# Optimization experiments

Measured on AMD Instinct MI355X. Metric: run time of the kernel, lower is better.

Reference implementation:

```python
import jax, jax.numpy as jnp
import numpy as np

THRESHOLD = 6.2
N_SECTIONS = 9      # n_conv_sections
SEC_LEN = 4         # n_section_length
SEC_H = 9           # n_input_sections + n_section_length - 1
BATCH = 16384


def setup_inputs() -> dict:
    key = jax.random.key(0)
    k1, k2 = jax.random.split(key)
    # input spike-wave tensor [T, C=1, H=41, W=40]
    x = jax.random.uniform(k1, (BATCH, 1, 41, 40), dtype=jnp.float32)
    # per-section conv weights, N(0.8, 0.05) as in snn.Convolution init
    W = 0.8 + 0.05 * jax.random.normal(k2, (N_SECTIONS, 50, 1, 6, 40), dtype=jnp.float32)
    return {"x": x, "W": W}


def _conv(sec, w):
    # sec: [B,1,9,40], w: [50,1,6,40] -> [B,50,4,1]
    return jax.lax.conv_general_dilated(
        sec, w, window_strides=(1, 1), padding='VALID',
        dimension_numbers=('NCHW', 'OIHW', 'NCHW'))


def reference(x, W):
    # slice the 9 overlapping input sections -> [9, B, 1, 9, 40]
    sec = jnp.stack([x[:, :, i * SEC_LEN:i * SEC_LEN + SEC_H, :]
                     for i in range(N_SECTIONS)])
    pots = jax.vmap(_conv)(sec, W)                      # [9, B, 50, 4, 1]
    pots = jnp.max(pots, axis=3, keepdims=True)         # Pooling((4,1)) -> [9, B, 50, 1, 1]
    spks = jnp.where(pots > THRESHOLD, 1.0, 0.0).astype(pots.dtype)
    # concat sections along height (dim=2 of [B,C,H,W])
    pots_cat = jnp.moveaxis(pots[:, :, :, 0, :], 0, 2)  # [B, 50, 9, 1]
    spks_cat = jnp.moveaxis(spks[:, :, :, 0, :], 0, 2)  # [B, 50, 9, 1]
    return pots_cat, spks_cat
```

## Files before the change

kernel.cpp:

```cpp
#include <hip/hip_runtime.h>
#include <cstdint>
#include <cstddef>

#define NBATCH   16384
#define NSEC     9
#define NOC      50
#define NOCP     64
#define KPAD     256
#define KREAL    240
#define XROW     1640
#define XSF      1664
#define TB       16
#define OUTHALF  7372800
#define THRESH   6.2f

typedef _Float16 half8  __attribute__((ext_vector_type(8)));
typedef float    f32x4  __attribute__((ext_vector_type(4)));

__device__ inline half8 cvt8(float4 a, float4 b) {
    half8 h;
    h[0] = (_Float16)a.x; h[1] = (_Float16)a.y;
    h[2] = (_Float16)a.z; h[3] = (_Float16)a.w;
    h[4] = (_Float16)b.x; h[5] = (_Float16)b.y;
    h[6] = (_Float16)b.z; h[7] = (_Float16)b.w;
    return h;
}

__device__ inline void stg_load(const float* __restrict__ xrow, int u,
                                float4& a, float4& b) {
    if (u < 205) {
        a = *(const float4*)(xrow + u * 8);
        b = *(const float4*)(xrow + u * 8 + 4);
    } else {
        a = float4{0, 0, 0, 0};
        b = float4{0, 0, 0, 0};
    }
}

__device__ inline void stg_write(_Float16* lrow, int u, int ssw,
                                 float4 a, float4 b) {
    *(half8*)(lrow + ((u ^ ssw) << 3)) = cvt8(a, b);
}

__global__ __launch_bounds__(256)
void wconv_kernel(const float* __restrict__ W, _Float16* __restrict__ wks) {
    int idx = blockIdx.x * 256 + threadIdx.x;
    int k   = idx & 255;
    int ocp = (idx >> 8) & 63;
    int sec = idx >> 14;
    float v = 0.0f;
    if (ocp < NOC && k < KREAL)
        v = W[(size_t)(sec * NOC + ocp) * KREAL + k];
    wks[idx] = (_Float16)v;
}

__global__ __launch_bounds__(256, 2)
void fused_kernel(const float* __restrict__ x,
                  const _Float16* __restrict__ wks,
                  float* __restrict__ out) {
    __shared__ __align__(16) _Float16 xs[TB * XSF];

    const int tid = threadIdx.x;
    const size_t b0 = (size_t)blockIdx.x * TB;

    const int bb  = tid >> 4;
    const int u16 = tid & 15;
    const int ssw = bb & 7;
    const float* xrow = x + (b0 + bb) * XROW;
    _Float16* lrow = xs + bb * XSF;

    const int lane  = tid & 63;
    const int w     = tid >> 6;
    const int l15   = lane & 15;
    const int quad  = lane >> 4;
    const int mbase = 8 * (w >> 1);
    const int nbase = 32 * (w & 1);

    const int row0 = mbase + (l15 >> 2);
    const int row1 = row0 + 4;
    const _Float16* arow0 = xs + row0 * XSF;
    const _Float16* arow1 = xs + row1 * XSF;
    const int sw0 = row0 & 7;
    const int sw1 = row1 & 7;
    const int ubase = (l15 & 3) * 5 + quad;

    const _Float16* wb = wks + (size_t)(nbase + l15) * KPAD + quad * 8;

    half8 bv0[2][4], bv1[2][4];
    f32x4 acc00, acc01, acc10, acc11;
    float res[NSEC][2][2];

#define BPREF(ss, hh, B) { \
    const _Float16* wsec_ = wb + (size_t)((ss) * NOCP) * KPAD + (hh) * 128; \
    B[0][0] = *(const half8*)(wsec_);                \
    B[0][1] = *(const half8*)(wsec_ + 32);           \
    B[0][2] = *(const half8*)(wsec_ + 64);           \
    B[0][3] = *(const half8*)(wsec_ + 96);           \
    B[1][0] = *(const half8*)(wsec_ + 16 * KPAD);        \
    B[1][1] = *(const half8*)(wsec_ + 16 * KPAD + 32);   \
    B[1][2] = *(const half8*)(wsec_ + 16 * KPAD + 64);   \
    B[1][3] = *(const half8*)(wsec_ + 16 * KPAD + 96);   \
}

#define CHALF(ss, hh, B) { \
    _Pragma("unroll") \
    for (int kk = 0; kk < 4; ++kk) { \
        const int unit_ = (ss) * 20 + ((hh) * 4 + kk) * 4 + ubase; \
        half8 av0_ = *(const half8*)(arow0 + ((unit_ ^ sw0) << 3)); \
        half8 av1_ = *(const half8*)(arow1 + ((unit_ ^ sw1) << 3)); \
        acc00 = __builtin_amdgcn_mfma_f32_16x16x32_f16(av0_, B[0][kk], acc00, 0, 0, 0); \
        acc01 = __builtin_amdgcn_mfma_f32_16x16x32_f16(av0_, B[1][kk], acc01, 0, 0, 0); \
        acc10 = __builtin_amdgcn_mfma_f32_16x16x32_f16(av1_, B[0][kk], acc10, 0, 0, 0); \
        acc11 = __builtin_amdgcn_mfma_f32_16x16x32_f16(av1_, B[1][kk], acc11, 0, 0, 0); \
    } \
}

#define SECTION(ss) { \
    BPREF(ss, 1, bv1); \
    acc00 = f32x4{}; acc01 = f32x4{}; acc10 = f32x4{}; acc11 = f32x4{}; \
    CHALF(ss, 0, bv0); \
    if ((ss) < 8) BPREF((ss) + 1, 0, bv0); \
    CHALF(ss, 1, bv1); \
    res[ss][0][0] = fmaxf(fmaxf(acc00[0], acc00[1]), fmaxf(acc00[2], acc00[3])); \
    res[ss][0][1] = fmaxf(fmaxf(acc01[0], acc01[1]), fmaxf(acc01[2], acc01[3])); \
    res[ss][1][0] = fmaxf(fmaxf(acc10[0], acc10[1]), fmaxf(acc10[2], acc10[3])); \
    res[ss][1][1] = fmaxf(fmaxf(acc11[0], acc11[1]), fmaxf(acc11[2], acc11[3])); \
}

    {
        #pragma unroll
        for (int c = 0; c < 2; ++c) {
            const int jn = c ? 6 : 7;
            float4 va[7], vb[7];
            #pragma unroll
            for (int jj = 0; jj < 7; ++jj)
                if (jj < jn)
                    stg_load(xrow, u16 + 16 * (c * 7 + jj), va[jj], vb[jj]);
            if (c == 0) BPREF(0, 0, bv0);
            #pragma unroll
            for (int jj = 0; jj < 7; ++jj)
                if (jj < jn)
                    stg_write(lrow, u16 + 16 * (c * 7 + jj), ssw, va[jj], vb[jj]);
        }
    }
    __syncthreads();

    SECTION(0);
    SECTION(1);
    SECTION(2);
    SECTION(3);
    SECTION(4);
    SECTION(5);
    SECTION(6);
    SECTION(7);
    SECTION(8);

    __syncthreads();
    float* tb = (float*)xs;
    #pragma unroll
    for (int mt = 0; mt < 2; ++mt) {
        const int bl = mbase + 4 * mt + quad;
        #pragma unroll
        for (int nt = 0; nt < 2; ++nt) {
            const int oc = nbase + nt * 16 + l15;
            if (oc < NOC) {
                #pragma unroll
                for (int s = 0; s < NSEC; ++s)
                    tb[bl * 450 + oc * 9 + s] = res[s][mt][nt];
            }
        }
    }
    __syncthreads();

    const size_t ob = b0 * 450;
    const float4* t4 = (const float4*)tb;
    float4* o4  = (float4*)(out + ob);
    float4* o4s = (float4*)(out + OUTHALF + ob);
    for (int i = tid; i < TB * 450 / 4; i += 256) {
        float4 v = t4[i];
        o4[i] = v;
        float4 sp;
        sp.x = (v.x > THRESH) ? 1.0f : 0.0f;
        sp.y = (v.y > THRESH) ? 1.0f : 0.0f;
        sp.z = (v.z > THRESH) ? 1.0f : 0.0f;
        sp.w = (v.w > THRESH) ? 1.0f : 0.0f;
        o4s[i] = sp;
    }
}

__global__ __launch_bounds__(256)
void naive_kernel(const float* __restrict__ x, const float* __restrict__ W,
                  float* __restrict__ out) {
    size_t idx = (size_t)blockIdx.x * 256 + threadIdx.x;
    if (idx >= OUTHALF) return;
    int s  = (int)(idx % NSEC);
    int oc = (int)((idx / NSEC) % NOC);
    int b  = (int)(idx / (NSEC * NOC));
    const float* xb = x + (size_t)b * XROW + s * 160;
    const float* wv = W + (size_t)(s * NOC + oc) * KREAL;
    float best = -1e30f;
    for (int h0 = 0; h0 < 4; ++h0) {
        float acc = 0.0f;
        for (int k = 0; k < KREAL; ++k)
            acc += xb[h0 * 40 + k] * wv[k];
        best = fmaxf(best, acc);
    }
    out[idx] = best;
    out[OUTHALF + idx] = (best > THRESH) ? 1.0f : 0.0f;
}

extern "C" void kernel_launch(void* const* d_in, const int* in_sizes, int n_in,
                              void* d_out, int out_size, void* d_ws, size_t ws_size,
                              hipStream_t stream) {
    const float* x = (const float*)d_in[0];
    const float* W = (const float*)d_in[1];
    float* out = (float*)d_out;

    const size_t w_bytes = (size_t)NSEC * NOCP * KPAD * sizeof(_Float16);

    if (ws_size < w_bytes) {
        naive_kernel<<<(OUTHALF + 255) / 256, 256, 0, stream>>>(x, W, out);
        return;
    }

    _Float16* wks = (_Float16*)d_ws;

    wconv_kernel<<<(NSEC * NOCP * KPAD) / 256, 256, 0, stream>>>(W, wks);
    fused_kernel<<<NBATCH / TB, 256, 0, stream>>>(x, wks, out);
}
```

Measured before the change: 229.8 us.

## Halve batch tile to 8 and split waves by output-channel block

Reduces the per-block batch tile from 16 to 8 samples and remaps the four waves so each wave owns one 16-channel block over all 8 samples, instead of a 2x2 split. This cuts per-thread accumulators and prefetched weight registers, halves LDS per block, and raises the launch-bounds occupancy hint to 4 blocks per SM while doubling the grid. In exchange, each weight fragment is reused across fewer samples, so weight traffic per output roughly doubles, and the staging loads are reorganized for 32 threads per row.

```diff
diff --git a/kernel.cpp b/kernel.cpp
--- a/kernel.cpp
+++ b/kernel.cpp
@@ -10,7 +10,7 @@
 #define KREAL    240
 #define XROW     1640
 #define XSF      1664
-#define TB       16
+#define TB       8
 #define OUTHALF  7372800
 #define THRESH   6.2f
 
@@ -54,7 +54,7 @@
     wks[idx] = (_Float16)v;
 }
 
-__global__ __launch_bounds__(256, 2)
+__global__ __launch_bounds__(256, 4)
 void fused_kernel(const float* __restrict__ x,
                   const _Float16* __restrict__ wks,
                   float* __restrict__ out) {
@@ -63,8 +63,8 @@
     const int tid = threadIdx.x;
     const size_t b0 = (size_t)blockIdx.x * TB;
 
-    const int bb  = tid >> 4;
-    const int u16 = tid & 15;
+    const int bb  = tid >> 5;
+    const int u32 = tid & 31;
     const int ssw = bb & 7;
     const float* xrow = x + (b0 + bb) * XROW;
     _Float16* lrow = xs + bb * XSF;
@@ -73,10 +73,8 @@
     const int w     = tid >> 6;
     const int l15   = lane & 15;
     const int quad  = lane >> 4;
-    const int mbase = 8 * (w >> 1);
-    const int nbase = 32 * (w & 1);
-
-    const int row0 = mbase + (l15 >> 2);
+
+    const int row0 = l15 >> 2;
     const int row1 = row0 + 4;
     const _Float16* arow0 = xs + row0 * XSF;
     const _Float16* arow1 = xs + row1 * XSF;
@@ -84,22 +82,19 @@
     const int sw1 = row1 & 7;
     const int ubase = (l15 & 3) * 5 + quad;
 
-    const _Float16* wb = wks + (size_t)(nbase + l15) * KPAD + quad * 8;
-
-    half8 bv0[2][4], bv1[2][4];
-    f32x4 acc00, acc01, acc10, acc11;
-    float res[NSEC][2][2];
+    const _Float16* wb = wks + (size_t)(w * 16 + l15) * KPAD + quad * 8;
+    const int oc = w * 16 + l15;
+
+    half8 bv0[4], bv1[4];
+    f32x4 acc0, acc1;
+    float res[NSEC][2];
 
 #define BPREF(ss, hh, B) { \
     const _Float16* wsec_ = wb + (size_t)((ss) * NOCP) * KPAD + (hh) * 128; \
-    B[0][0] = *(const half8*)(wsec_);                \
-    B[0][1] = *(const half8*)(wsec_ + 32);           \
-    B[0][2] = *(const half8*)(wsec_ + 64);           \
-    B[0][3] = *(const half8*)(wsec_ + 96);           \
-    B[1][0] = *(const half8*)(wsec_ + 16 * KPAD);        \
-    B[1][1] = *(const half8*)(wsec_ + 16 * KPAD + 32);   \
-    B[1][2] = *(const half8*)(wsec_ + 16 * KPAD + 64);   \
-    B[1][3] = *(const half8*)(wsec_ + 16 * KPAD + 96);   \
+    B[0] = *(const half8*)(wsec_);        \
+    B[1] = *(const half8*)(wsec_ + 32);   \
+    B[2] = *(const half8*)(wsec_ + 64);   \
+    B[3] = *(const half8*)(wsec_ + 96);   \
 }
 
 #define CHALF(ss, hh, B) { \
@@ -108,40 +103,40 @@
         const int unit_ = (ss) * 20 + ((hh) * 4 + kk) * 4 + ubase; \
         half8 av0_ = *(const half8*)(arow0 + ((unit_ ^ sw0) << 3)); \
         half8 av1_ = *(const half8*)(arow1 + ((unit_ ^ sw1) << 3)); \
-        acc00 = __builtin_amdgcn_mfma_f32_16x16x32_f16(av0_, B[0][kk], acc00, 0, 0, 0); \
-        acc01 = __builtin_amdgcn_mfma_f32_16x16x32_f16(av0_, B[1][kk], acc01, 0, 0, 0); \
-        acc10 = __builtin_amdgcn_mfma_f32_16x16x32_f16(av1_, B[0][kk], acc10, 0, 0, 0); \
-        acc11 = __builtin_amdgcn_mfma_f32_16x16x32_f16(av1_, B[1][kk], acc11, 0, 0, 0); \
+        acc0 = __builtin_amdgcn_mfma_f32_16x16x32_f16(av0_, B[kk], acc0, 0, 0, 0); \
+        acc1 = __builtin_amdgcn_mfma_f32_16x16x32_f16(av1_, B[kk], acc1, 0, 0, 0); \
     } \
 }
 
 #define SECTION(ss) { \
     BPREF(ss, 1, bv1); \
-    acc00 = f32x4{}; acc01 = f32x4{}; acc10 = f32x4{}; acc11 = f32x4{}; \
+    acc0 = f32x4{}; acc1 = f32x4{}; \
     CHALF(ss, 0, bv0); \
     if ((ss) < 8) BPREF((ss) + 1, 0, bv0); \
     CHALF(ss, 1, bv1); \
-    res[ss][0][0] = fmaxf(fmaxf(acc00[0], acc00[1]), fmaxf(acc00[2], acc00[3])); \
-    res[ss][0][1] = fmaxf(fmaxf(acc01[0], acc01[1]), fmaxf(acc01[2], acc01[3])); \
-    res[ss][1][0] = fmaxf(fmaxf(acc10[0], acc10[1]), fmaxf(acc10[2], acc10[3])); \
-    res[ss][1][1] = fmaxf(fmaxf(acc11[0], acc11[1]), fmaxf(acc11[2], acc11[3])); \
+    res[ss][0] = fmaxf(fmaxf(acc0[0], acc0[1]), fmaxf(acc0[2], acc0[3])); \
+    res[ss][1] = fmaxf(fmaxf(acc1[0], acc1[1]), fmaxf(acc1[2], acc1[3])); \
 }
 
     {
-        #pragma unroll
-        for (int c = 0; c < 2; ++c) {
-            const int jn = c ? 6 : 7;
-            float4 va[7], vb[7];
-            #pragma unroll
-            for (int jj = 0; jj < 7; ++jj)
-                if (jj < jn)
-                    stg_load(xrow, u16 + 16 * (c * 7 + jj), va[jj], vb[jj]);
-            if (c == 0) BPREF(0, 0, bv0);
-            #pragma unroll
-            for (int jj = 0; jj < 7; ++jj)
-                if (jj < jn)
-                    stg_write(lrow, u16 + 16 * (c * 7 + jj), ssw, va[jj], vb[jj]);
-        }
+        float4 va[4], vb[4];
+        #pragma unroll
+        for (int j = 0; j < 4; ++j)
+            stg_load(xrow, u32 + 32 * j, va[j], vb[j]);
+        BPREF(0, 0, bv0);
+        #pragma unroll
+        for (int j = 0; j < 4; ++j)
+            stg_write(lrow, u32 + 32 * j, ssw, va[j], vb[j]);
+        #pragma unroll
+        for (int j = 4; j < 6; ++j)
+            stg_load(xrow, u32 + 32 * j, va[j - 4], vb[j - 4]);
+        if (u32 < 16)
+            stg_load(xrow, u32 + 192, va[2], vb[2]);
+        #pragma unroll
+        for (int j = 4; j < 6; ++j)
+            stg_write(lrow, u32 + 32 * j, ssw, va[j - 4], vb[j - 4]);
+        if (u32 < 16)
+            stg_write(lrow, u32 + 192, ssw, va[2], vb[2]);
     }
     __syncthreads();
 
@@ -157,17 +152,13 @@
 
     __syncthreads();
     float* tb = (float*)xs;
-    #pragma unroll
-    for (int mt = 0; mt < 2; ++mt) {
-        const int bl = mbase + 4 * mt + quad;
-        #pragma unroll
-        for (int nt = 0; nt < 2; ++nt) {
-            const int oc = nbase + nt * 16 + l15;
-            if (oc < NOC) {
-                #pragma unroll
-                for (int s = 0; s < NSEC; ++s)
-                    tb[bl * 450 + oc * 9 + s] = res[s][mt][nt];
-            }
+    if (oc < NOC) {
+        #pragma unroll
+        for (int mt = 0; mt < 2; ++mt) {
+            const int bl = mt * 4 + quad;
+            #pragma unroll
+            for (int s = 0; s < NSEC; ++s)
+                tb[bl * 450 + oc * 9 + s] = res[s][mt];
         }
     }
     __syncthreads();
```

Result: faster. 223.3 us (-2.8%).
